# Kernel tuning notes

Hardware: AMD Instinct MI355X
Metric: run time of the kernel (lower is better)

Reference implementation:

```python
import jax, jax.numpy as jnp
import numpy as np

N = 2048          # batch
T = 50            # max_num_visit
CODES = 40        # codes per visit
VOCAB = 527       # max_tokens for CategoryEncoding
MH = VOCAB - 1    # 526 after dropping column 0
AUX = 10          # aux_info feature dim
E = 256           # config.embedding_dim (LSTM units)


def setup_inputs() -> dict:
    key = jax.random.key(0)
    ks = jax.random.split(key, 10)
    code = jax.random.randint(ks[0], (N, T, CODES), 0, VOCAB, dtype=jnp.int32)
    aux_info = jax.random.normal(ks[1], (N, T, AUX), jnp.float32)
    length = jax.random.randint(ks[2], (N,), 1, T + 1, dtype=jnp.int32)

    def glorot(k, shape):
        fan = shape[0]
        return jax.random.normal(k, shape, jnp.float32) * (1.0 / np.sqrt(fan))

    W_lin = glorot(ks[3], (MH + AUX, E)); b_lin = jnp.zeros((E,), jnp.float32)
    K_lstm = glorot(ks[4], (E, 4 * E))
    R_lstm = glorot(ks[5], (E, 4 * E))
    b_lstm = jnp.zeros((4 * E,), jnp.float32)
    W0 = glorot(ks[6], (E, 256)); b0 = jnp.zeros((256,), jnp.float32)
    W1 = glorot(ks[7], (256, 256)); b1 = jnp.zeros((256,), jnp.float32)
    return dict(code=code, aux_info=aux_info, length=length, is_training=0,
                W_lin=W_lin, b_lin=b_lin, K_lstm=K_lstm, R_lstm=R_lstm,
                b_lstm=b_lstm, W0=W0, b0=b0, W1=W1, b1=b1)


def _multi_hot(code):
    # CategoryEncoding binary mode: presence indicator over vocab, drop col 0
    flat = code.reshape(N * T, CODES)
    mh = jnp.zeros((N * T, VOCAB), jnp.float32)
    mh = mh.at[jnp.arange(N * T)[:, None], flat].set(1.0)
    return mh[:, 1:].reshape(N, T, MH)


def _lstm(x, K, R, b):
    # Keras LSTM, gate order [i, f, g(c), o]; inference (dropout off)
    xz = jnp.einsum('nte,eh->nth', x, K) + b          # [N,T,4E]
    xz = jnp.transpose(xz, (1, 0, 2))                  # [T,N,4E]

    def step(carry, zt):
        h, c = carry
        z = zt + h @ R
        i, f, g, o = jnp.split(z, 4, axis=-1)
        c = jax.nn.sigmoid(f) * c + jax.nn.sigmoid(i) * jnp.tanh(g)
        h = jax.nn.sigmoid(o) * jnp.tanh(c)
        return (h, c), h

    h0 = jnp.zeros((N, E), jnp.float32)
    (_, _), hs = jax.lax.scan(step, (h0, h0), xz)
    return jnp.transpose(hs, (1, 0, 2))                # [N,T,E]


def reference(code, aux_info, length, is_training,
              W_lin, b_lin, K_lstm, R_lstm, b_lstm, W0, b0, W1, b1):
    mh = _multi_hot(code)                              # [N,T,526]
    x = jax.nn.relu(jnp.concatenate([mh, aux_info], axis=-1) @ W_lin + b_lin)
    h = _lstm(x, K_lstm, R_lstm, b_lstm)               # [N,T,E]
    x_last = h[jnp.arange(N), length - 1]              # gather_nd: last valid step
    fv = jax.nn.relu(x_last @ W0 + b0) @ W1 + b1
    fv = fv / jnp.sqrt(jnp.sum(fv ** 2, axis=-1, keepdims=True))
    return fv
```

## Files before the change

### kernel.cpp

```cpp
#include <hip/hip_runtime.h>
#include <hip/hip_bf16.h>
#include <math.h>
#include <stdint.h>

#define N_BATCH 2048
#define T_STEPS 50
#define NCODES  40
#define MH      526
#define AUXD    10
#define WLROWS  536
#define E_DIM   256
#define G_DIM   1024
#define TCHUNK  10
#define MBLK    64
#define NFUSED  (TCHUNK * 32)

typedef __attribute__((ext_vector_type(8))) short short8;
typedef __attribute__((ext_vector_type(4))) short short4v;
typedef __attribute__((ext_vector_type(4))) float f32x4;
typedef __attribute__((ext_vector_type(4))) int   i32x4;

__device__ __forceinline__ short f2bf(float f) {
    __hip_bfloat16 h = __float2bfloat16(f);
    return *reinterpret_cast<short*>(&h);
}
__device__ __forceinline__ float bf2f(unsigned short u) {
    return __uint_as_float(((unsigned int)u) << 16);
}
__device__ __forceinline__ float sigf(float x) {
    return 1.f / (1.f + __expf(-x));
}
__device__ __forceinline__ float tanhfast(float x) {
    return 2.f / (1.f + __expf(-2.f * x)) - 1.f;
}

__global__ __launch_bounds__(256) void k_zero(int* __restrict__ cnt)
{
    const int i = blockIdx.x * 256 + threadIdx.x;
    if (i < 64 * 32) cnt[i] = 0;
}

__global__ __launch_bounds__(256) void k_prep_wcoop(
    const float* __restrict__ R, short* __restrict__ Wcoop)
{
    const int gid  = blockIdx.x * 256 + threadIdx.x;
    const int fg   = gid >> 6, lane = gid & 63;
    const int p    = lane >> 4, lr = lane & 15;
    const int kk   = fg & 7;
    const int g    = (fg >> 3) & 3;
    const int w    = (fg >> 5) & 3;
    const int cs   = fg >> 7;
    const int n    = g * 256 + cs * 64 + w * 16 + lr;
    short* dst = Wcoop + (size_t)fg * 512 + lane * 8;
    #pragma unroll
    for (int j = 0; j < 8; ++j)
        dst[j] = f2bf(R[(size_t)(kk * 32 + p * 8 + j) * G_DIM + n]);
}

__global__ __launch_bounds__(256) void k_prep_wfk(
    const float* __restrict__ K, short* __restrict__ WfK)
{
    const int gid  = blockIdx.x * 256 + threadIdx.x;
    const int fg   = gid >> 6, lane = gid & 63;
    const int p    = lane >> 4, lr = lane & 15;
    const int kb   = fg >> 6;
    const int cb   = (fg >> 3) & 7;
    const int w    = fg & 7;
    const int n    = w * 128 + cb * 16 + lr;
    short* dst = WfK + (size_t)fg * 512 + lane * 8;
    #pragma unroll
    for (int j = 0; j < 8; ++j)
        dst[j] = f2bf(K[(size_t)(kb * 32 + p * 8 + j) * G_DIM + n]);
}

__global__ __launch_bounds__(256) void k_prep_wfl(
    const float* __restrict__ W_lin, short* __restrict__ WfL)
{
    const int gid  = blockIdx.x * 256 + threadIdx.x;
    const int fg   = gid >> 6, lane = gid & 63;
    const int p    = lane >> 4, lr = lane & 15;
    const int kk   = fg >> 4;
    const int cb   = (fg >> 3) & 1;
    const int w    = fg & 7;
    const int n    = w * 32 + cb * 16 + lr;
    short* dst = WfL + (size_t)fg * 512 + lane * 8;
    #pragma unroll
    for (int j = 0; j < 8; ++j) {
        const int k = kk * 32 + p * 8 + j;
        dst[j] = (k < WLROWS) ? f2bf(W_lin[(size_t)k * E_DIM + n]) : (short)0;
    }
}

__global__ __launch_bounds__(512, 1) void k_fused(
    const int* __restrict__ code, const float* __restrict__ aux,
    const short* __restrict__ WfL, const float* __restrict__ b_lin,
    const short* __restrict__ WfK, short* __restrict__ xzp, int t0f)
{
    const int tid  = threadIdx.x;
    const int w    = tid >> 6;
    const int lane = tid & 63;
    const int lr   = lane & 15;
    const int p    = lane >> 4;
    const int fid  = blockIdx.x;
    const int tl   = fid >> 5;
    const int ngg  = fid & 31;
    const int n0   = ngg * MBLK;
    const int t    = t0f + tl;
    const int ph8  = (fid >> 3) & 7;
    const int ph17 = (fid >> 3) % 17;

    __shared__ __align__(16) short oh[MBLK][552];
    __shared__ __align__(16) short xs[MBLK][264];

    for (int i = tid; i < (MBLK * 552) / 8; i += 512)
        ((int4*)&oh[0][0])[i] = (int4){0, 0, 0, 0};
    __syncthreads();

    for (int i = tid; i < MBLK * NCODES; i += 512) {
        const int r = i / NCODES;
        const int j = i - r * NCODES;
        const int c = code[((size_t)(n0 + r) * T_STEPS + t) * NCODES + j];
        if (c > 0) ((unsigned short*)&oh[0][0])[r * 552 + (c - 1)] = 0x3F80;
    }
    for (int i = tid; i < MBLK * AUXD; i += 512) {
        const int r = i / AUXD;
        const int a = i - r * AUXD;
        oh[r][MH + a] = f2bf(aux[((size_t)(n0 + r) * T_STEPS + t) * AUXD + a]);
    }
    __syncthreads();

    const short* wfl_thr = WfL + (size_t)w * 512 + lane * 8;
    const short* wfk_thr = WfK + (size_t)w * 512 + lane * 8;

    {
        f32x4 acc[4][2];
        #pragma unroll
        for (int rb = 0; rb < 4; ++rb)
            #pragma unroll
            for (int cb = 0; cb < 2; ++cb)
                acc[rb][cb] = (f32x4){0.f, 0.f, 0.f, 0.f};

        for (int kk = 0; kk < 17; ++kk) {
            int kx = kk + ph17; if (kx >= 17) kx -= 17;
            short8 a[4];
            #pragma unroll
            for (int rb = 0; rb < 4; ++rb)
                a[rb] = *(const short8*)&oh[rb * 16 + lr][kx * 32 + p * 8];
            #pragma unroll
            for (int cb = 0; cb < 2; ++cb) {
                short8 bf = *(const short8*)(wfl_thr + (size_t)(kx * 2 + cb) * 4096);
                #pragma unroll
                for (int rb = 0; rb < 4; ++rb)
                    acc[rb][cb] = __builtin_amdgcn_mfma_f32_16x16x32_bf16(
                        a[rb], bf, acc[rb][cb], 0, 0, 0);
            }
        }
        float bias[2];
        #pragma unroll
        for (int cb = 0; cb < 2; ++cb) bias[cb] = b_lin[w * 32 + cb * 16 + lr];
        #pragma unroll
        for (int rb = 0; rb < 4; ++rb)
            #pragma unroll
            for (int cb = 0; cb < 2; ++cb)
                #pragma unroll
                for (int rr = 0; rr < 4; ++rr)
                    xs[rb * 16 + p * 4 + rr][w * 32 + cb * 16 + lr] =
                        f2bf(fmaxf(acc[rb][cb][rr] + bias[cb], 0.f));
        __syncthreads();
    }

    #pragma unroll
    for (int half = 0; half < 2; ++half) {
        f32x4 acc[4][4];
        #pragma unroll
        for (int rb = 0; rb < 4; ++rb)
            #pragma unroll
            for (int c4 = 0; c4 < 4; ++c4)
                acc[rb][c4] = (f32x4){0.f, 0.f, 0.f, 0.f};

        for (int kb = 0; kb < 8; ++kb) {
            const int kx = (kb + ph8) & 7;
            short8 a[4];
            #pragma unroll
            for (int rb = 0; rb < 4; ++rb)
                a[rb] = *(const short8*)&xs[rb * 16 + lr][kx * 32 + p * 8];
            #pragma unroll
            for (int c4 = 0; c4 < 4; ++c4) {
                const int cb = half * 4 + c4;
                short8 bf = *(const short8*)(wfk_thr + (size_t)(kx * 8 + cb) * 4096);
                #pragma unroll
                for (int rb = 0; rb < 4; ++rb)
                    acc[rb][c4] = __builtin_amdgcn_mfma_f32_16x16x32_bf16(
                        a[rb], bf, acc[rb][c4], 0, 0, 0);
            }
        }
        #pragma unroll
        for (int rb = 0; rb < 4; ++rb) {
            const int rgg = ngg * 4 + rb;
            #pragma unroll
            for (int c4 = 0; c4 < 4; ++c4) {
                const int cb = half * 4 + c4;
                const int c0 = w * 128 + cb * 16;
                const int g  = c0 >> 8;
                const int wp = (c0 >> 5) & 7;
                const int eb = (c0 >> 4) & 1;
                const int j8 = eb * 4 + g;
                short4v v;
                #pragma unroll
                for (int rr = 0; rr < 4; ++rr) v[rr] = f2bf(acc[rb][c4][rr]);
                *(short4v*)(xzp +
                    (((size_t)rgg * TCHUNK + tl) * 64 + wp * 8 + j8) * 256 +
                    lane * 4) = v;
            }
        }
    }
}

__global__ __launch_bounds__(256, 1) void k_rcoop(
    const short* __restrict__ xzp, const int* __restrict__ length,
    const short* __restrict__ Wcoop, const float* __restrict__ b,
    short* __restrict__ h_buf, float* __restrict__ c_state,
    float* __restrict__ xlast, int* __restrict__ flags,
    int t0, int bar_base)
{
    const int tid  = threadIdx.x;
    const int w    = tid >> 6;
    const int lane = tid & 63;
    const int lr   = lane & 15;
    const int p    = lane >> 4;
    const int cs   = blockIdx.x >> 6;
    const int rg   = blockIdx.x & 63;
    const int r0   = rg * 32;
    const int e    = cs * 64 + w * 16 + lr;

    __shared__ __align__(16) short h_o[32][64];
    __shared__ int s_len[32];
    if (tid < 32) s_len[tid] = length[r0 + tid];

    short8 bw[4][8];
    {
        const short* wb = Wcoop + ((size_t)((cs * 4 + w) * 4)) * 8 * 512 + lane * 8;
        #pragma unroll
        for (int g = 0; g < 4; ++g)
            #pragma unroll
            for (int kk = 0; kk < 8; ++kk)
                bw[g][kk] = *(const short8*)(wb + (size_t)(g * 8 + kk) * 512);
    }

    float bias[4];
    #pragma unroll
    for (int g = 0; g < 4; ++g) bias[g] = b[g * 256 + e];

    float creg[2][4];
    if (t0 == 0) {
        #pragma unroll
        for (int rf = 0; rf < 2; ++rf)
            #pragma unroll
            for (int rr = 0; rr < 4; ++rr) creg[rf][rr] = 0.f;
    } else {
        #pragma unroll
        for (int rf = 0; rf < 2; ++rf)
            #pragma unroll
            for (int rr = 0; rr < 4; ++rr)
                creg[rf][rr] = c_state[(size_t)(r0 + rf * 16 + p * 4 + rr) * E_DIM + e];
    }
    __syncthreads();

    int len_r[2][4];
    #pragma unroll
    for (int rf = 0; rf < 2; ++rf)
        #pragma unroll
        for (int rr = 0; rr < 4; ++rr)
            len_r[rf][rr] = s_len[rf * 16 + p * 4 + rr];

    int* flag = flags + rg * 32;
    int bcnt = bar_base;

#define PEERS_BARRIER()                                                        \
    do {                                                                       \
        ++bcnt;                                                                \
        __syncthreads();             \
        if (tid == 0) {                                                        \
            __hip_atomic_fetch_add(flag, 1, __ATOMIC_RELAXED,                  \
                                   __HIP_MEMORY_SCOPE_AGENT);                  \
            while (__hip_atomic_load(flag, __ATOMIC_RELAXED,                   \
                                     __HIP_MEMORY_SCOPE_AGENT) < 4 * bcnt)     \
                __builtin_amdgcn_s_sleep(1);                                   \
        }                                                                      \
        __syncthreads();                                                       \
    } while (0)

    if (t0 == 0) {
        const i32x4 z4 = {0, 0, 0, 0};
        const int row = tid >> 3, seg = tid & 7;
        const uint64_t dst = (uint64_t)(uintptr_t)(h_buf +
            (size_t)(r0 + row) * E_DIM + cs * 64 + seg * 8);
        asm volatile("global_store_dwordx4 %0, %1, off sc0 sc1"
                     :: "v"(dst), "v"(z4) : "memory");
        PEERS_BARRIER();
    }

    short4v xv[2][4];
    #pragma unroll
    for (int rf = 0; rf < 2; ++rf)
        #pragma unroll
        for (int g = 0; g < 4; ++g)
            xv[rf][g] = *(const short4v*)(xzp +
                (((size_t)(2 * rg + rf) * TCHUNK + 0) * 64 +
                 (cs * 2 + (w >> 1)) * 8 + (w & 1) * 4 + g) * 256 + lane * 4);

    for (int tl = 0; tl < TCHUNK; ++tl) {
        const int t = t0 + tl;
        const short* hb_r = h_buf + (size_t)(t & 1) * (N_BATCH * E_DIM);

        short8 a[2][8];
        #pragma unroll
        for (int rf = 0; rf < 2; ++rf) {
            const uint64_t base = (uint64_t)(uintptr_t)(hb_r +
                (size_t)(r0 + rf * 16 + lr) * E_DIM + p * 8);
            asm volatile(
                "global_load_dwordx4 %0, %8, off sc0 sc1\n\t"
                "global_load_dwordx4 %1, %8, off offset:64 sc0 sc1\n\t"
                "global_load_dwordx4 %2, %8, off offset:128 sc0 sc1\n\t"
                "global_load_dwordx4 %3, %8, off offset:192 sc0 sc1\n\t"
                "global_load_dwordx4 %4, %8, off offset:256 sc0 sc1\n\t"
                "global_load_dwordx4 %5, %8, off offset:320 sc0 sc1\n\t"
                "global_load_dwordx4 %6, %8, off offset:384 sc0 sc1\n\t"
                "global_load_dwordx4 %7, %8, off offset:448 sc0 sc1"
                : "=&v"(a[rf][0]), "=&v"(a[rf][1]), "=&v"(a[rf][2]), "=&v"(a[rf][3]),
                  "=&v"(a[rf][4]), "=&v"(a[rf][5]), "=&v"(a[rf][6]), "=&v"(a[rf][7])
                : "v"(base));
        }

        f32x4 acc[2][4];
        #pragma unroll
        for (int rf = 0; rf < 2; ++rf)
            #pragma unroll
            for (int g = 0; g < 4; ++g)
                #pragma unroll
                for (int rr = 0; rr < 4; ++rr)
                    acc[rf][g][rr] = bf2f((unsigned short)xv[rf][g][rr]);

        asm volatile("s_waitcnt vmcnt(0)" ::: "memory");
        __builtin_amdgcn_sched_barrier(0);

        #pragma unroll
        for (int kk = 0; kk < 8; ++kk)
            #pragma unroll
            for (int g = 0; g < 4; ++g)
                #pragma unroll
                for (int rf = 0; rf < 2; ++rf)
                    acc[rf][g] = __builtin_amdgcn_mfma_f32_16x16x32_bf16(
                        a[rf][kk], bw[g][kk], acc[rf][g], 0, 0, 0);

        if (tl + 1 < TCHUNK) {
            #pragma unroll
            for (int rf = 0; rf < 2; ++rf)
                #pragma unroll
                for (int g = 0; g < 4; ++g)
                    xv[rf][g] = *(const short4v*)(xzp +
                        (((size_t)(2 * rg + rf) * TCHUNK + tl + 1) * 64 +
                         (cs * 2 + (w >> 1)) * 8 + (w & 1) * 4 + g) * 256 + lane * 4);
        }

        #pragma unroll
        for (int rf = 0; rf < 2; ++rf) {
            #pragma unroll
            for (int rr = 0; rr < 4; ++rr) {
                float zi = acc[rf][0][rr] + bias[0];
                float zf = acc[rf][1][rr] + bias[1];
                float zg = acc[rf][2][rr] + bias[2];
                float zo = acc[rf][3][rr] + bias[3];
                float ig = sigf(zi), fg = sigf(zf);
                float gg = tanhfast(zg), og = sigf(zo);
                float cc = fg * creg[rf][rr] + ig * gg;
                float hh = og * tanhfast(cc);
                creg[rf][rr] = cc;
                h_o[rf * 16 + p * 4 + rr][w * 16 + lr] = f2bf(hh);
                const int row = r0 + rf * 16 + p * 4 + rr;
                if (t == len_r[rf][rr] - 1)
                    xlast[(size_t)row * E_DIM + e] = hh;
            }
        }
        __syncthreads();

        {
            short* hb_w = h_buf + (size_t)((t + 1) & 1) * (N_BATCH * E_DIM);
            const int row = tid >> 3, seg = tid & 7;
            i32x4 v = *(const i32x4*)&h_o[row][seg * 8];
            const uint64_t dst = (uint64_t)(uintptr_t)(hb_w +
                (size_t)(r0 + row) * E_DIM + cs * 64 + seg * 8);
            asm volatile("global_store_dwordx4 %0, %1, off sc0 sc1"
                         :: "v"(dst), "v"(v) : "memory");
        }

        if (tl + 1 < TCHUNK) PEERS_BARRIER();
    }

    #pragma unroll
    for (int rf = 0; rf < 2; ++rf)
        #pragma unroll
        for (int rr = 0; rr < 4; ++rr)
            c_state[(size_t)(r0 + rf * 16 + p * 4 + rr) * E_DIM + e] = creg[rf][rr];
#undef PEERS_BARRIER
}

__global__ __launch_bounds__(256) void k_head(
    const float* __restrict__ xlast,
    const float* __restrict__ W0, const float* __restrict__ b0,
    const float* __restrict__ W1, const float* __restrict__ b1,
    float* __restrict__ out)
{
    const int n = blockIdx.x;
    const int j = threadIdx.x;

    __shared__ __align__(16) float xsh[E_DIM];
    __shared__ __align__(16) float y0[E_DIM];
    __shared__ float part[4];

    xsh[j] = xlast[(size_t)n * E_DIM + j];
    __syncthreads();

    float acc = b0[j];
    for (int k4 = 0; k4 < E_DIM; k4 += 4) {
        float4 xv = *reinterpret_cast<const float4*>(&xsh[k4]);
        #pragma unroll
        for (int kk = 0; kk < 4; ++kk)
            acc += (&xv.x)[kk] * W0[(size_t)(k4 + kk) * E_DIM + j];
    }
    y0[j] = fmaxf(acc, 0.f);
    __syncthreads();

    acc = b1[j];
    for (int k4 = 0; k4 < E_DIM; k4 += 4) {
        float4 yv = *reinterpret_cast<const float4*>(&y0[k4]);
        #pragma unroll
        for (int kk = 0; kk < 4; ++kk)
            acc += (&yv.x)[kk] * W1[(size_t)(k4 + kk) * E_DIM + j];
    }

    float sq = acc * acc;
    #pragma unroll
    for (int off = 32; off > 0; off >>= 1)
        sq += __shfl_xor(sq, off, 64);
    if ((j & 63) == 0) part[j >> 6] = sq;
    __syncthreads();
    float total = part[0] + part[1] + part[2] + part[3];

    out[(size_t)n * E_DIM + j] = acc * rsqrtf(total);
}

extern "C" void kernel_launch(void* const* d_in, const int* in_sizes, int n_in,
                              void* d_out, int out_size, void* d_ws, size_t ws_size,
                              hipStream_t stream) {
    const int*   code   = (const int*)  d_in[0];
    const float* aux    = (const float*)d_in[1];
    const int*   length = (const int*)  d_in[2];
    const float* W_lin  = (const float*)d_in[4];
    const float* b_lin  = (const float*)d_in[5];
    const float* K      = (const float*)d_in[6];
    const float* R      = (const float*)d_in[7];
    const float* b      = (const float*)d_in[8];
    const float* W0     = (const float*)d_in[9];
    const float* b0     = (const float*)d_in[10];
    const float* W1     = (const float*)d_in[11];
    const float* b1     = (const float*)d_in[12];
    float* out = (float*)d_out;

    char* ws = (char*)d_ws;
    short* Wcoop   = (short*)(ws + 0);
    short* WfK     = (short*)(ws + 524288);
    short* WfL     = (short*)(ws + 1048576);
    float* xlast   = (float*)(ws + 1327104);
    float* c_state = (float*)(ws + 3424256);
    short* h_buf   = (short*)(ws + 5521408);
    int*   flags   = (int*)  (ws + 7618560);
    short* xzp     = (short*)(ws + 7634944);

    k_zero      <<<8,   256, 0, stream>>>(flags);
    k_prep_wcoop<<<128, 256, 0, stream>>>(R, Wcoop);
    k_prep_wfk  <<<128, 256, 0, stream>>>(K, WfK);
    k_prep_wfl  <<<68,  256, 0, stream>>>(W_lin, WfL);

    for (int c = 0; c < T_STEPS / TCHUNK; ++c) {
        const int t0 = c * TCHUNK;
        const int bar_base = (c == 0) ? 0 : 1 + 9 * c;
        k_fused<<<NFUSED, 512, 0, stream>>>(code, aux, WfL, b_lin, WfK, xzp, t0);
        k_rcoop<<<256, 256, 0, stream>>>(xzp, length, Wcoop, b, h_buf,
                                         c_state, xlast, flags, t0, bar_base);
    }

    k_head<<<N_BATCH, 256, 0, stream>>>(xlast, W0, b0, W1, b1, out);
}
```

Baseline: 497.6 us.

## Overlap input projection of next chunk with recurrent LSTM chunk in one kernel

Merges the input-projection kernel and the cooperative recurrent kernel into a single combo launch. The first blocks run the recurrence for chunk c while the remaining blocks compute the projection for chunk c+1 into a double-buffered xz buffer, so the two stages can overlap instead of alternating serially. The projection tile is also halved to 32 rows (twice as many blocks), and the spin barrier drops s_sleep. Risks: the recurrent blocks rely on a spin barrier among co-resident peers, so if the fused blocks occupy CUs first the recurrence can stall or deadlock. Recurrent blocks now launch with 512 threads, half of them idle.

```diff
diff --git a/kernel.cpp b/kernel.cpp
--- a/kernel.cpp
+++ b/kernel.cpp
@@ -12,8 +12,9 @@
 #define E_DIM   256
 #define G_DIM   1024
 #define TCHUNK  10
-#define MBLK    64
-#define NFUSED  (TCHUNK * 32)
+#define MBLK    32
+#define NFUSED  (TCHUNK * 64)
+#define NRCOOP  256
 
 typedef __attribute__((ext_vector_type(8))) short short8;
 typedef __attribute__((ext_vector_type(4))) short short4v;
@@ -91,26 +92,26 @@
     }
 }
 
-__global__ __launch_bounds__(512, 1) void k_fused(
+__device__ __forceinline__ void fused_body(
+    int fid, short* smem,
     const int* __restrict__ code, const float* __restrict__ aux,
     const short* __restrict__ WfL, const float* __restrict__ b_lin,
-    const short* __restrict__ WfK, short* __restrict__ xzp, int t0f)
+    const short* __restrict__ WfK, short* __restrict__ xz_w, int t0f)
 {
     const int tid  = threadIdx.x;
     const int w    = tid >> 6;
     const int lane = tid & 63;
     const int lr   = lane & 15;
     const int p    = lane >> 4;
-    const int fid  = blockIdx.x;
-    const int tl   = fid >> 5;
-    const int ngg  = fid & 31;
+    const int tl   = fid >> 6;
+    const int ngg  = fid & 63;
     const int n0   = ngg * MBLK;
     const int t    = t0f + tl;
     const int ph8  = (fid >> 3) & 7;
     const int ph17 = (fid >> 3) % 17;
 
-    __shared__ __align__(16) short oh[MBLK][552];
-    __shared__ __align__(16) short xs[MBLK][264];
+    short (*oh)[552] = (short (*)[552])smem;
+    short (*xs)[264] = (short (*)[264])(smem + MBLK * 552);
 
     for (int i = tid; i < (MBLK * 552) / 8; i += 512)
         ((int4*)&oh[0][0])[i] = (int4){0, 0, 0, 0};
@@ -122,9 +123,9 @@
         const int c = code[((size_t)(n0 + r) * T_STEPS + t) * NCODES + j];
         if (c > 0) ((unsigned short*)&oh[0][0])[r * 552 + (c - 1)] = 0x3F80;
     }
-    for (int i = tid; i < MBLK * AUXD; i += 512) {
-        const int r = i / AUXD;
-        const int a = i - r * AUXD;
+    if (tid < MBLK * AUXD) {
+        const int r = tid / AUXD;
+        const int a = tid - r * AUXD;
         oh[r][MH + a] = f2bf(aux[((size_t)(n0 + r) * T_STEPS + t) * AUXD + a]);
     }
     __syncthreads();
@@ -133,33 +134,29 @@
     const short* wfk_thr = WfK + (size_t)w * 512 + lane * 8;
 
     {
-        f32x4 acc[4][2];
-        #pragma unroll
-        for (int rb = 0; rb < 4; ++rb)
+        f32x4 acc[2][2];
+        #pragma unroll
+        for (int rb = 0; rb < 2; ++rb)
             #pragma unroll
             for (int cb = 0; cb < 2; ++cb)
                 acc[rb][cb] = (f32x4){0.f, 0.f, 0.f, 0.f};
 
         for (int kk = 0; kk < 17; ++kk) {
             int kx = kk + ph17; if (kx >= 17) kx -= 17;
-            short8 a[4];
-            #pragma unroll
-            for (int rb = 0; rb < 4; ++rb)
-                a[rb] = *(const short8*)&oh[rb * 16 + lr][kx * 32 + p * 8];
+            short8 a0 = *(const short8*)&oh[lr][kx * 32 + p * 8];
+            short8 a1 = *(const short8*)&oh[16 + lr][kx * 32 + p * 8];
             #pragma unroll
             for (int cb = 0; cb < 2; ++cb) {
                 short8 bf = *(const short8*)(wfl_thr + (size_t)(kx * 2 + cb) * 4096);
-                #pragma unroll
-                for (int rb = 0; rb < 4; ++rb)
-                    acc[rb][cb] = __builtin_amdgcn_mfma_f32_16x16x32_bf16(
-                        a[rb], bf, acc[rb][cb], 0, 0, 0);
+                acc[0][cb] = __builtin_amdgcn_mfma_f32_16x16x32_bf16(a0, bf, acc[0][cb], 0, 0, 0);
+                acc[1][cb] = __builtin_amdgcn_mfma_f32_16x16x32_bf16(a1, bf, acc[1][cb], 0, 0, 0);
             }
         }
         float bias[2];
         #pragma unroll
         for (int cb = 0; cb < 2; ++cb) bias[cb] = b_lin[w * 32 + cb * 16 + lr];
         #pragma unroll
-        for (int rb = 0; rb < 4; ++rb)
+        for (int rb = 0; rb < 2; ++rb)
             #pragma unroll
             for (int cb = 0; cb < 2; ++cb)
                 #pragma unroll
@@ -169,37 +166,33 @@
         __syncthreads();
     }
 
-    #pragma unroll
-    for (int half = 0; half < 2; ++half) {
-        f32x4 acc[4][4];
-        #pragma unroll
-        for (int rb = 0; rb < 4; ++rb)
-            #pragma unroll
-            for (int c4 = 0; c4 < 4; ++c4)
-                acc[rb][c4] = (f32x4){0.f, 0.f, 0.f, 0.f};
+    {
+        f32x4 acc[2][8];
+        #pragma unroll
+        for (int rb = 0; rb < 2; ++rb)
+            #pragma unroll
+            for (int cb = 0; cb < 8; ++cb)
+                acc[rb][cb] = (f32x4){0.f, 0.f, 0.f, 0.f};
 
         for (int kb = 0; kb < 8; ++kb) {
             const int kx = (kb + ph8) & 7;
-            short8 a[4];
-            #pragma unroll
-            for (int rb = 0; rb < 4; ++rb)
-                a[rb] = *(const short8*)&xs[rb * 16 + lr][kx * 32 + p * 8];
-            #pragma unroll
-            for (int c4 = 0; c4 < 4; ++c4) {
-                const int cb = half * 4 + c4;
-                short8 bf = *(const short8*)(wfk_thr + (size_t)(kx * 8 + cb) * 4096);
-                #pragma unroll
-                for (int rb = 0; rb < 4; ++rb)
-                    acc[rb][c4] = __builtin_amdgcn_mfma_f32_16x16x32_bf16(
-                        a[rb], bf, acc[rb][c4], 0, 0, 0);
+            short8 a0 = *(const short8*)&xs[lr][kx * 32 + p * 8];
+            short8 a1 = *(const short8*)&xs[16 + lr][kx * 32 + p * 8];
+            short8 bf[8];
+            #pragma unroll
+            for (int cb = 0; cb < 8; ++cb)
+                bf[cb] = *(const short8*)(wfk_thr + (size_t)(kx * 8 + cb) * 4096);
+            #pragma unroll
+            for (int cb = 0; cb < 8; ++cb) {
+                acc[0][cb] = __builtin_amdgcn_mfma_f32_16x16x32_bf16(a0, bf[cb], acc[0][cb], 0, 0, 0);
+                acc[1][cb] = __builtin_amdgcn_mfma_f32_16x16x32_bf16(a1, bf[cb], acc[1][cb], 0, 0, 0);
             }
         }
         #pragma unroll
-        for (int rb = 0; rb < 4; ++rb) {
-            const int rgg = ngg * 4 + rb;
-            #pragma unroll
-            for (int c4 = 0; c4 < 4; ++c4) {
-                const int cb = half * 4 + c4;
+        for (int rb = 0; rb < 2; ++rb) {
+            const int rgg = ngg * 2 + rb;
+            #pragma unroll
+            for (int cb = 0; cb < 8; ++cb) {
                 const int c0 = w * 128 + cb * 16;
                 const int g  = c0 >> 8;
                 const int wp = (c0 >> 5) & 7;
@@ -207,8 +200,8 @@
                 const int j8 = eb * 4 + g;
                 short4v v;
                 #pragma unroll
-                for (int rr = 0; rr < 4; ++rr) v[rr] = f2bf(acc[rb][c4][rr]);
-                *(short4v*)(xzp +
+                for (int rr = 0; rr < 4; ++rr) v[rr] = f2bf(acc[rb][cb][rr]);
+                *(short4v*)(xz_w +
                     (((size_t)rgg * TCHUNK + tl) * 64 + wp * 8 + j8) * 256 +
                     lane * 4) = v;
             }
@@ -216,7 +209,8 @@
     }
 }
 
-__global__ __launch_bounds__(256, 1) void k_rcoop(
+__device__ __forceinline__ void rcoop_body(
+    int bid, short* smem, int* s_len,
     const short* __restrict__ xzp, const int* __restrict__ length,
     const short* __restrict__ Wcoop, const float* __restrict__ b,
     short* __restrict__ h_buf, float* __restrict__ c_state,
@@ -224,17 +218,18 @@
     int t0, int bar_base)
 {
     const int tid  = threadIdx.x;
-    const int w    = tid >> 6;
+    const bool act = tid < 256;
+    const int w    = (tid >> 6) & 3;
     const int lane = tid & 63;
     const int lr   = lane & 15;
     const int p    = lane >> 4;
-    const int cs   = blockIdx.x >> 6;
-    const int rg   = blockIdx.x & 63;
+    const int cs   = bid >> 6;
+    const int rg   = bid & 63;
     const int r0   = rg * 32;
     const int e    = cs * 64 + w * 16 + lr;
 
-    __shared__ __align__(16) short h_o[32][64];
-    __shared__ int s_len[32];
+    short (*h_o)[64] = (short (*)[64])smem;
+
     if (tid < 32) s_len[tid] = length[r0 + tid];
 
     short8 bw[4][8];
@@ -279,24 +274,25 @@
 #define PEERS_BARRIER()                                                        \
     do {                                                                       \
         ++bcnt;                                                                \
-        __syncthreads();             \
+        __syncthreads();                 \
         if (tid == 0) {                                                        \
             __hip_atomic_fetch_add(flag, 1, __ATOMIC_RELAXED,                  \
                                    __HIP_MEMORY_SCOPE_AGENT);                  \
             while (__hip_atomic_load(flag, __ATOMIC_RELAXED,                   \
-                                     __HIP_MEMORY_SCOPE_AGENT) < 4 * bcnt)     \
-                __builtin_amdgcn_s_sleep(1);                                   \
+                                     __HIP_MEMORY_SCOPE_AGENT) < 4 * bcnt) {}  \
         }                                                                      \
         __syncthreads();                                                       \
     } while (0)
 
     if (t0 == 0) {
-        const i32x4 z4 = {0, 0, 0, 0};
-        const int row = tid >> 3, seg = tid & 7;
-        const uint64_t dst = (uint64_t)(uintptr_t)(h_buf +
-            (size_t)(r0 + row) * E_DIM + cs * 64 + seg * 8);
-        asm volatile("global_store_dwordx4 %0, %1, off sc0 sc1"
-                     :: "v"(dst), "v"(z4) : "memory");
+        if (act) {
+            const i32x4 z4 = {0, 0, 0, 0};
+            const int row = tid >> 3, seg = tid & 7;
+            const uint64_t dst = (uint64_t)(uintptr_t)(h_buf +
+                (size_t)(r0 + row) * E_DIM + cs * 64 + seg * 8);
+            asm volatile("global_store_dwordx4 %0, %1, off sc0 sc1"
+                         :: "v"(dst), "v"(z4) : "memory");
+        }
         PEERS_BARRIER();
     }
 
@@ -376,15 +372,17 @@
                 float cc = fg * creg[rf][rr] + ig * gg;
                 float hh = og * tanhfast(cc);
                 creg[rf][rr] = cc;
-                h_o[rf * 16 + p * 4 + rr][w * 16 + lr] = f2bf(hh);
-                const int row = r0 + rf * 16 + p * 4 + rr;
-                if (t == len_r[rf][rr] - 1)
-                    xlast[(size_t)row * E_DIM + e] = hh;
+                if (act) {
+                    h_o[rf * 16 + p * 4 + rr][w * 16 + lr] = f2bf(hh);
+                    const int row = r0 + rf * 16 + p * 4 + rr;
+                    if (t == len_r[rf][rr] - 1)
+                        xlast[(size_t)row * E_DIM + e] = hh;
+                }
             }
         }
         __syncthreads();
 
-        {
+        if (act) {
             short* hb_w = h_buf + (size_t)((t + 1) & 1) * (N_BATCH * E_DIM);
             const int row = tid >> 3, seg = tid & 7;
             i32x4 v = *(const i32x4*)&h_o[row][seg * 8];
@@ -397,12 +395,37 @@
         if (tl + 1 < TCHUNK) PEERS_BARRIER();
     }
 
-    #pragma unroll
-    for (int rf = 0; rf < 2; ++rf)
-        #pragma unroll
-        for (int rr = 0; rr < 4; ++rr)
-            c_state[(size_t)(r0 + rf * 16 + p * 4 + rr) * E_DIM + e] = creg[rf][rr];
+    if (act) {
+        #pragma unroll
+        for (int rf = 0; rf < 2; ++rf)
+            #pragma unroll
+            for (int rr = 0; rr < 4; ++rr)
+                c_state[(size_t)(r0 + rf * 16 + p * 4 + rr) * E_DIM + e] = creg[rf][rr];
+    }
 #undef PEERS_BARRIER
+}
+
+__global__ __launch_bounds__(512, 1) void k_combo(
+    const int* __restrict__ code, const float* __restrict__ aux,
+    const short* __restrict__ WfL, const float* __restrict__ b_lin,
+    const short* __restrict__ WfK,
+    const short* __restrict__ Wcoop, const float* __restrict__ b,
+    const int* __restrict__ length,
+    short* __restrict__ h_buf, float* __restrict__ c_state,
+    float* __restrict__ xlast, int* __restrict__ flags,
+    const short* __restrict__ xz_r, short* __restrict__ xz_w,
+    int t0r, int t0f, int rec_cnt, int bar_base)
+{
+    __shared__ __align__(16) short smem[26112];
+    __shared__ int s_len[64];
+    const int bid = blockIdx.x;
+    if (bid < rec_cnt) {
+        rcoop_body(bid, smem, s_len, xz_r, length, Wcoop, b,
+                   h_buf, c_state, xlast, flags, t0r, bar_base);
+    } else if (t0f >= 0) {
+        fused_body(bid - rec_cnt, smem, code, aux, WfL, b_lin, WfK,
+                   xz_w, t0f);
+    }
 }
 
 __global__ __launch_bounds__(256) void k_head(
@@ -475,20 +498,32 @@
     float* c_state = (float*)(ws + 3424256);
     short* h_buf   = (short*)(ws + 5521408);
     int*   flags   = (int*)  (ws + 7618560);
-    short* xzp     = (short*)(ws + 7634944);
+    short* xzp0    = (short*)(ws + 7634944);
+    short* xzp1    = (short*)(ws + 49577984);
 
     k_zero      <<<8,   256, 0, stream>>>(flags);
     k_prep_wcoop<<<128, 256, 0, stream>>>(R, Wcoop);
     k_prep_wfk  <<<128, 256, 0, stream>>>(K, WfK);
     k_prep_wfl  <<<68,  256, 0, stream>>>(W_lin, WfL);
 
-    for (int c = 0; c < T_STEPS / TCHUNK; ++c) {
-        const int t0 = c * TCHUNK;
-        const int bar_base = (c == 0) ? 0 : 1 + 9 * c;
-        k_fused<<<NFUSED, 512, 0, stream>>>(code, aux, WfL, b_lin, WfK, xzp, t0);
-        k_rcoop<<<256, 256, 0, stream>>>(xzp, length, Wcoop, b, h_buf,
-                                         c_state, xlast, flags, t0, bar_base);
-    }
+    short* xzbuf[2] = {xzp0, xzp1};
+
+    k_combo<<<NFUSED, 512, 0, stream>>>(
+        code, aux, WfL, b_lin, WfK, Wcoop, b, length,
+        h_buf, c_state, xlast, flags, xzp0, xzp0, 0, 0, 0, 0);
+
+    for (int c = 0; c < 4; ++c) {
+        const int bar_base = (c == 0) ? 0 : 9 * c + 1;
+        k_combo<<<NRCOOP + NFUSED, 512, 0, stream>>>(
+            code, aux, WfL, b_lin, WfK, Wcoop, b, length,
+            h_buf, c_state, xlast, flags,
+            xzbuf[c & 1], xzbuf[(c + 1) & 1],
+            c * TCHUNK, (c + 1) * TCHUNK, NRCOOP, bar_base);
+    }
+    k_combo<<<NRCOOP, 512, 0, stream>>>(
+        code, aux, WfL, b_lin, WfK, Wcoop, b, length,
+        h_buf, c_state, xlast, flags, xzbuf[0], xzbuf[0],
+        4 * TCHUNK, -1, NRCOOP, 9 * 4 + 1);
 
     k_head<<<N_BATCH, 256, 0, stream>>>(xlast, W0, b0, W1, b1, out);
 }
```

New measurement: 635.9 us. 27.8% more time.

## Double-buffer xz projections so each recurrent launch covers two chunks

Applied to the files above, without the earlier changes.

The input-projection kernel now writes into two alternating xz buffers. This lets the cooperative LSTM recurrence kernel run 20 timesteps per launch instead of 10, cutting the recurrent launches from five to three. Each launch gets its own zeroed flag region, so the barrier counter restarts at zero. The intent is to remove launch gaps and per-launch setup, such as reloading weights and c_state, in the serial recurrence. The cost is a second large workspace buffer and less interleaving between projection and recurrence.

```diff
diff --git a/kernel.cpp b/kernel.cpp
--- a/kernel.cpp
+++ b/kernel.cpp
@@ -37,7 +37,7 @@
 __global__ __launch_bounds__(256) void k_zero(int* __restrict__ cnt)
 {
     const int i = blockIdx.x * 256 + threadIdx.x;
-    if (i < 64 * 32) cnt[i] = 0;
+    if (i < 3 * 64 * 32) cnt[i] = 0;
 }
 
 __global__ __launch_bounds__(256) void k_prep_wcoop(
@@ -217,11 +217,12 @@
 }
 
 __global__ __launch_bounds__(256, 1) void k_rcoop(
-    const short* __restrict__ xzp, const int* __restrict__ length,
+    const short* __restrict__ xz0, const short* __restrict__ xz1,
+    const int* __restrict__ length,
     const short* __restrict__ Wcoop, const float* __restrict__ b,
     short* __restrict__ h_buf, float* __restrict__ c_state,
     float* __restrict__ xlast, int* __restrict__ flags,
-    int t0, int bar_base)
+    int t0, int nsteps)
 {
     const int tid  = threadIdx.x;
     const int w    = tid >> 6;
@@ -274,12 +275,12 @@
             len_r[rf][rr] = s_len[rf * 16 + p * 4 + rr];
 
     int* flag = flags + rg * 32;
-    int bcnt = bar_base;
+    int bcnt = 0;
 
 #define PEERS_BARRIER()                                                        \
     do {                                                                       \
         ++bcnt;                                                                \
-        __syncthreads();             \
+        __syncthreads();                 \
         if (tid == 0) {                                                        \
             __hip_atomic_fetch_add(flag, 1, __ATOMIC_RELAXED,                  \
                                    __HIP_MEMORY_SCOPE_AGENT);                  \
@@ -300,18 +301,31 @@
         PEERS_BARRIER();
     }
 
+    const short* hb0 = h_buf;
+    const short* hb1 = h_buf + (size_t)N_BATCH * E_DIM;
+    const size_t coloff = (size_t)((cs * 2 + (w >> 1)) * 8 + (w & 1) * 4) * 256 +
+                          lane * 4;
+    const size_t rowoff0 = (size_t)(2 * rg + 0) * TCHUNK * 16384;
+    const size_t rowoff1 = (size_t)(2 * rg + 1) * TCHUNK * 16384;
+
+#define XZ_BASE(T, RFOFF)                                                      \
+    ((((((T) / TCHUNK) & 1) ? xz1 : xz0)) + (RFOFF) +                          \
+     (size_t)((T) % TCHUNK) * 16384 + coloff)
+
     short4v xv[2][4];
-    #pragma unroll
-    for (int rf = 0; rf < 2; ++rf)
-        #pragma unroll
-        for (int g = 0; g < 4; ++g)
-            xv[rf][g] = *(const short4v*)(xzp +
-                (((size_t)(2 * rg + rf) * TCHUNK + 0) * 64 +
-                 (cs * 2 + (w >> 1)) * 8 + (w & 1) * 4 + g) * 256 + lane * 4);
-
-    for (int tl = 0; tl < TCHUNK; ++tl) {
-        const int t = t0 + tl;
-        const short* hb_r = h_buf + (size_t)(t & 1) * (N_BATCH * E_DIM);
+    {
+        const short* b0p = XZ_BASE(t0, rowoff0);
+        const short* b1p = XZ_BASE(t0, rowoff1);
+        #pragma unroll
+        for (int g = 0; g < 4; ++g) {
+            xv[0][g] = *(const short4v*)(b0p + g * 256);
+            xv[1][g] = *(const short4v*)(b1p + g * 256);
+        }
+    }
+
+    for (int s = 0; s < nsteps; ++s) {
+        const int t = t0 + s;
+        const short* hb_r = (t & 1) ? hb1 : hb0;
 
         short8 a[2][8];
         #pragma unroll
@@ -353,14 +367,14 @@
                     acc[rf][g] = __builtin_amdgcn_mfma_f32_16x16x32_bf16(
                         a[rf][kk], bw[g][kk], acc[rf][g], 0, 0, 0);
 
-        if (tl + 1 < TCHUNK) {
-            #pragma unroll
-            for (int rf = 0; rf < 2; ++rf)
-                #pragma unroll
-                for (int g = 0; g < 4; ++g)
-                    xv[rf][g] = *(const short4v*)(xzp +
-                        (((size_t)(2 * rg + rf) * TCHUNK + tl + 1) * 64 +
-                         (cs * 2 + (w >> 1)) * 8 + (w & 1) * 4 + g) * 256 + lane * 4);
+        if (s + 1 < nsteps) {
+            const short* b0p = XZ_BASE(t + 1, rowoff0);
+            const short* b1p = XZ_BASE(t + 1, rowoff1);
+            #pragma unroll
+            for (int g = 0; g < 4; ++g) {
+                xv[0][g] = *(const short4v*)(b0p + g * 256);
+                xv[1][g] = *(const short4v*)(b1p + g * 256);
+            }
         }
 
         #pragma unroll
@@ -385,7 +399,7 @@
         __syncthreads();
 
         {
-            short* hb_w = h_buf + (size_t)((t + 1) & 1) * (N_BATCH * E_DIM);
+            short* hb_w = (short*)(((t + 1) & 1) ? hb1 : hb0);
             const int row = tid >> 3, seg = tid & 7;
             i32x4 v = *(const i32x4*)&h_o[row][seg * 8];
             const uint64_t dst = (uint64_t)(uintptr_t)(hb_w +
@@ -394,7 +408,7 @@
                          :: "v"(dst), "v"(v) : "memory");
         }
 
-        if (tl + 1 < TCHUNK) PEERS_BARRIER();
+        if (s + 1 < nsteps) PEERS_BARRIER();
     }
 
     #pragma unroll
@@ -403,6 +417,7 @@
         for (int rr = 0; rr < 4; ++rr)
             c_state[(size_t)(r0 + rf * 16 + p * 4 + rr) * E_DIM + e] = creg[rf][rr];
 #undef PEERS_BARRIER
+#undef XZ_BASE
 }
 
 __global__ __launch_bounds__(256) void k_head(
@@ -475,20 +490,25 @@
     float* c_state = (float*)(ws + 3424256);
     short* h_buf   = (short*)(ws + 5521408);
     int*   flags   = (int*)  (ws + 7618560);
-    short* xzp     = (short*)(ws + 7634944);
-
-    k_zero      <<<8,   256, 0, stream>>>(flags);
+    short* xzp0    = (short*)(ws + 7643136);
+    short* xzp1    = (short*)(ws + 49586176);
+
+    k_zero      <<<24,  256, 0, stream>>>(flags);
     k_prep_wcoop<<<128, 256, 0, stream>>>(R, Wcoop);
     k_prep_wfk  <<<128, 256, 0, stream>>>(K, WfK);
     k_prep_wfl  <<<68,  256, 0, stream>>>(W_lin, WfL);
 
-    for (int c = 0; c < T_STEPS / TCHUNK; ++c) {
-        const int t0 = c * TCHUNK;
-        const int bar_base = (c == 0) ? 0 : 1 + 9 * c;
-        k_fused<<<NFUSED, 512, 0, stream>>>(code, aux, WfL, b_lin, WfK, xzp, t0);
-        k_rcoop<<<256, 256, 0, stream>>>(xzp, length, Wcoop, b, h_buf,
-                                         c_state, xlast, flags, t0, bar_base);
-    }
+    k_fused<<<NFUSED, 512, 0, stream>>>(code, aux, WfL, b_lin, WfK, xzp0, 0);
+    k_fused<<<NFUSED, 512, 0, stream>>>(code, aux, WfL, b_lin, WfK, xzp1, 10);
+    k_rcoop<<<256, 256, 0, stream>>>(xzp0, xzp1, length, Wcoop, b, h_buf,
+                                     c_state, xlast, flags + 0 * 2048, 0, 20);
+    k_fused<<<NFUSED, 512, 0, stream>>>(code, aux, WfL, b_lin, WfK, xzp0, 20);
+    k_fused<<<NFUSED, 512, 0, stream>>>(code, aux, WfL, b_lin, WfK, xzp1, 30);
+    k_rcoop<<<256, 256, 0, stream>>>(xzp0, xzp1, length, Wcoop, b, h_buf,
+                                     c_state, xlast, flags + 1 * 2048, 20, 20);
+    k_fused<<<NFUSED, 512, 0, stream>>>(code, aux, WfL, b_lin, WfK, xzp0, 40);
+    k_rcoop<<<256, 256, 0, stream>>>(xzp0, xzp1, length, Wcoop, b, h_buf,
+                                     c_state, xlast, flags + 2 * 2048, 40, 10);
 
     k_head<<<N_BATCH, 256, 0, stream>>>(xlast, W0, b0, W1, b1, out);
 }
```

Measured after the change: 478.2 us. 3.9% less time.
